# Optimization experiments

Measured on AMD Instinct MI355X. Metric: run time of the kernel, lower is better.

Reference implementation:

```python
import jax, jax.numpy as jnp
import numpy as np

B, TE, TD, H, D = 8, 2048, 256, 128, 128


def setup_inputs() -> dict:
    key = jax.random.key(0)
    k1, k2, k3, k4, k5 = jax.random.split(key, 5)
    he = lambda k, shape: jax.random.normal(k, shape, dtype=jnp.float32) * jnp.sqrt(2.0 / shape[0])
    return {
        "encoder_out_seq": jax.random.normal(k1, (B, TE, H), dtype=jnp.float32),
        "decoder_out_seq": jax.random.normal(k2, (B, TD, D), dtype=jnp.float32),
        "W_a": he(k3, (H, H)),
        "U_a": he(k4, (D, H)),
        "V_a": he(k5, (H, 1)),
    }


def reference(encoder_out_seq, decoder_out_seq, W_a, U_a, V_a):
    # Precompute encoder and decoder projections once (the TF code redundantly
    # recomputes enc@W_a every decoder step inside backend.rnn).
    Wenc = jnp.einsum('bth,hk->btk', encoder_out_seq, W_a)      # [B,Te,H]
    Udec = jnp.einsum('bjd,dk->bjk', decoder_out_seq, U_a)     # [B,Td,H]
    # Additive (Bahdanau) scores: v^T tanh(W s_i + U h_j)
    scores = jnp.einsum('bjtk,k->bjt',
                        jnp.tanh(Wenc[:, None, :, :] + Udec[:, :, None, :]),
                        V_a[:, 0])                              # [B,Td,Te]
    e_outputs = jax.nn.softmax(scores, axis=-1)                 # [B,Td,Te]
    c_outputs = jnp.einsum('bjt,bth->bjh', e_outputs, encoder_out_seq)  # [B,Td,H]
    return c_outputs, e_outputs
```

## Files before the change

kernel.cpp:

```cpp
#include <hip/hip_runtime.h>
#include <stdint.h>

#define B  8
#define TE 2048
#define TD 256
#define H  128

#define FMA4(acc, s, wv) \
  acc.x += (s)*(wv).x; acc.y += (s)*(wv).y; acc.z += (s)*(wv).z; acc.w += (s)*(wv).w

__global__ __launch_bounds__(256) void proj_kernel(
    const float* __restrict__ enc, const float* __restrict__ dec,
    const float* __restrict__ Wa,  const float* __restrict__ Ua,
    float* __restrict__ EgT, float* __restrict__ Fg) {
  __shared__ float Ls[16 * 132];
  const float C2 = 2.8853900817779268f;
  int tid = threadIdx.x;
  int bid = blockIdx.x;
  bool isE = (bid < 1024);
  int rbase = (isE ? bid : bid - 1024) * 16;
  const float* in = isE ? enc : dec;
  const float* Mg = isE ? Wa : Ua;
  int hq = tid & 31, rq = tid >> 5;
  int h0 = hq * 4, r0 = rq * 2;
  const float* rowp = in + (size_t)(rbase + r0) * H;
  const float* wp = Mg + h0;
  float4 a0{0,0,0,0}, a1{0,0,0,0};
  #pragma unroll 2
  for (int kb = 0; kb < 32; ++kb) {
    float4 rv0 = *(const float4*)(rowp + kb * 4);
    float4 rv1 = *(const float4*)(rowp + H + kb * 4);
    float4 w0 = *(const float4*)(wp + (size_t)(4 * kb + 0) * H);
    float4 w1 = *(const float4*)(wp + (size_t)(4 * kb + 1) * H);
    float4 w2 = *(const float4*)(wp + (size_t)(4 * kb + 2) * H);
    float4 w3 = *(const float4*)(wp + (size_t)(4 * kb + 3) * H);
    FMA4(a0, rv0.x, w0); FMA4(a0, rv0.y, w1); FMA4(a0, rv0.z, w2); FMA4(a0, rv0.w, w3);
    FMA4(a1, rv1.x, w0); FMA4(a1, rv1.y, w1); FMA4(a1, rv1.z, w2); FMA4(a1, rv1.w, w3);
  }
  float4 e0, e1;
  e0.x = __builtin_amdgcn_exp2f(a0.x * C2); e0.y = __builtin_amdgcn_exp2f(a0.y * C2);
  e0.z = __builtin_amdgcn_exp2f(a0.z * C2); e0.w = __builtin_amdgcn_exp2f(a0.w * C2);
  e1.x = __builtin_amdgcn_exp2f(a1.x * C2); e1.y = __builtin_amdgcn_exp2f(a1.y * C2);
  e1.z = __builtin_amdgcn_exp2f(a1.z * C2); e1.w = __builtin_amdgcn_exp2f(a1.w * C2);
  if (isE) {
    *(float4*)&Ls[(r0 + 0) * 132 + h0] = e0;
    *(float4*)&Ls[(r0 + 1) * 132 + h0] = e1;
    __syncthreads();
    int b_e = rbase >> 11, t_in = rbase & 2047;
    int tb = t_in >> 6, toff = t_in & 63;
    float* dst = EgT + (size_t)(b_e * 32 + tb) * 8192 + toff * 2;
    #pragma unroll
    for (int jj = 0; jj < 4; ++jj) {
      int idx = jj * 256 + tid;
      int r = idx & 15, q = idx >> 4;
      float2 val{Ls[r * 132 + 2 * q], Ls[r * 132 + 2 * q + 1]};
      *(float2*)(dst + (size_t)q * 128 + r * 2) = val;
    }
  } else {
    int b_f = rbase >> 8, j_in = rbase & 255;
    float* dst = Fg + ((size_t)(b_f * TD + j_in + r0)) * H + h0;
    *(float4*)(dst + 0 * H) = e0;
    *(float4*)(dst + 1 * H) = e1;
  }
}

__global__ __launch_bounds__(512, 4) void fused_kernel(
    const float* __restrict__ EgT, const float* __restrict__ Fg,
    const float* __restrict__ Va,  const float* __restrict__ enc,
    float* __restrict__ oute, float* __restrict__ outc) {
  __shared__ float S[4 * 2048];
  __shared__ float red[16];
  int tid = threadIdx.x;
  int bid = blockIdx.x;
  int b = bid & 7, jt = bid >> 3;
  int j0 = jt * 4;
  int lane = tid & 63, w = tid >> 6;
  const float4* vp = (const float4*)Va;
  float V1 = 0.f;
  #pragma unroll
  for (int q = 0; q < 32; ++q) { float4 v = vp[q]; V1 += v.x + v.y + v.z + v.w; }

  const float4* Fp = (const float4*)(Fg + (size_t)(b * TD + j0) * H);
  const float* Ep[4];
  #pragma unroll
  for (int it = 0; it < 4; ++it)
    Ep[it] = EgT + (size_t)(b * 32 + w + 8 * it) * 8192 + lane * 2;
  float s[4][4];
  #pragma unroll
  for (int it = 0; it < 4; ++it)
    #pragma unroll
    for (int j = 0; j < 4; ++j) s[it][j] = 0.f;
  float2 eka[4], ekb[4];

#define LOADE2(dst, base, off)                                       \
  { const float* _p = (base) + (off);                                \
    dst[0] = *(const float2*)(_p);       dst[1] = *(const float2*)(_p + 128);  \
    dst[2] = *(const float2*)(_p + 256); dst[3] = *(const float2*)(_p + 384); }

#define UNIT(acc, ekk, jj)                                                    \
  {                                                                           \
    float d0, d1, a = 0.f;                                                    \
    d0 = fmaf(ekk[0].x, f0[jj].x, 1.0f); d1 = fmaf(ekk[0].y, f0[jj].y, 1.0f); \
    a += (v0.x * d1 + v0.y * d0) * __builtin_amdgcn_rcpf(d0 * d1);            \
    d0 = fmaf(ekk[1].x, f0[jj].z, 1.0f); d1 = fmaf(ekk[1].y, f0[jj].w, 1.0f); \
    a += (v0.z * d1 + v0.w * d0) * __builtin_amdgcn_rcpf(d0 * d1);            \
    d0 = fmaf(ekk[2].x, f1[jj].x, 1.0f); d1 = fmaf(ekk[2].y, f1[jj].y, 1.0f); \
    a += (v1.x * d1 + v1.y * d0) * __builtin_amdgcn_rcpf(d0 * d1);            \
    d0 = fmaf(ekk[3].x, f1[jj].z, 1.0f); d1 = fmaf(ekk[3].y, f1[jj].w, 1.0f); \
    a += (v1.z * d1 + v1.w * d0) * __builtin_amdgcn_rcpf(d0 * d1);            \
    acc += a;                                                                 \
  }

  LOADE2(eka, Ep[0], 0);
  for (int kc = 0; kc < 16; ++kc) {
    float4 f0[4], f1[4];
    const float4* fpc = Fp + kc * 2;
    #pragma unroll
    for (int j = 0; j < 4; ++j) {
      f0[j] = fpc[j * 32];
      f1[j] = fpc[j * 32 + 1];
    }
    float4 v0 = vp[kc * 2], v1 = vp[kc * 2 + 1];
    LOADE2(ekb, Ep[1], kc * 512);
    #pragma unroll
    for (int j = 0; j < 4; ++j) UNIT(s[0][j], eka, j)
    LOADE2(eka, Ep[2], kc * 512);
    #pragma unroll
    for (int j = 0; j < 4; ++j) UNIT(s[1][j], ekb, j)
    LOADE2(ekb, Ep[3], kc * 512);
    #pragma unroll
    for (int j = 0; j < 4; ++j) UNIT(s[2][j], eka, j)
    LOADE2(eka, Ep[0], (kc + 1) * 512);
    #pragma unroll
    for (int j = 0; j < 4; ++j) UNIT(s[3][j], ekb, j)
  }
  #pragma unroll
  for (int it = 0; it < 4; ++it) {
    int t = (w + 8 * it) * 64 + lane;
    S[0 * 2048 + t] = V1 - 2.0f * s[it][0];
    S[1 * 2048 + t] = V1 - 2.0f * s[it][1];
    S[2 * 2048 + t] = V1 - 2.0f * s[it][2];
    S[3 * 2048 + t] = V1 - 2.0f * s[it][3];
  }
  __syncthreads();

  int j = w >> 1, half = w & 1;
  int tb2 = half * 1024 + lane;
  float x[16];
  #pragma unroll
  for (int q = 0; q < 16; ++q) x[q] = S[j * 2048 + tb2 + q * 64];
  float m = x[0];
  #pragma unroll
  for (int q = 1; q < 16; ++q) m = fmaxf(m, x[q]);
  #pragma unroll
  for (int off = 32; off > 0; off >>= 1) m = fmaxf(m, __shfl_xor(m, off));
  if (lane == 0) red[w] = m;
  __syncthreads();
  m = fmaxf(red[j * 2], red[j * 2 + 1]);
  const float L2E = 1.4426950408889634f;
  float sum = 0.f;
  #pragma unroll
  for (int q = 0; q < 16; ++q) {
    x[q] = __builtin_amdgcn_exp2f((x[q] - m) * L2E);
    sum += x[q];
  }
  #pragma unroll
  for (int off = 32; off > 0; off >>= 1) sum += __shfl_xor(sum, off);
  if (lane == 0) red[8 + w] = sum;
  __syncthreads();
  float inv = 1.0f / (red[8 + j * 2] + red[8 + j * 2 + 1]);
  float* orow = oute + (size_t)(b * TD + j0 + j) * TE;
  #pragma unroll
  for (int q = 0; q < 16; ++q) {
    float e = x[q] * inv;
    int t = tb2 + q * 64;
    orow[t] = e;
    S[j * 2048 + t] = e;
  }
  __syncthreads();

  int hq = tid & 31, slice = tid >> 5;
  const float* encp = enc + ((size_t)b * TE + slice * 128) * H + hq * 4;
  const float* Se = S + slice * 128;
  float4 ac0{0,0,0,0}, ac1{0,0,0,0}, ac2{0,0,0,0}, ac3{0,0,0,0};
  float4 evA0, evA1, evA2, evA3, evB0, evB1, evB2, evB3;

#define LOADENC(d0, d1, d2, d3, t0)                         \
  d0 = *(const float4*)(encp + (size_t)(t0 + 0) * H);       \
  d1 = *(const float4*)(encp + (size_t)(t0 + 1) * H);       \
  d2 = *(const float4*)(encp + (size_t)(t0 + 2) * H);       \
  d3 = *(const float4*)(encp + (size_t)(t0 + 3) * H);

#define GROUP(t0, ex, ey, ez, ew)                                            \
  {                                                                          \
    float4 E0 = *(const float4*)&Se[0 * 2048 + (t0)];                        \
    float4 E1 = *(const float4*)&Se[1 * 2048 + (t0)];                        \
    float4 E2 = *(const float4*)&Se[2 * 2048 + (t0)];                        \
    float4 E3 = *(const float4*)&Se[3 * 2048 + (t0)];                        \
    FMA4(ac0, E0.x, ex); FMA4(ac0, E0.y, ey); FMA4(ac0, E0.z, ez); FMA4(ac0, E0.w, ew); \
    FMA4(ac1, E1.x, ex); FMA4(ac1, E1.y, ey); FMA4(ac1, E1.z, ez); FMA4(ac1, E1.w, ew); \
    FMA4(ac2, E2.x, ex); FMA4(ac2, E2.y, ey); FMA4(ac2, E2.z, ez); FMA4(ac2, E2.w, ew); \
    FMA4(ac3, E3.x, ex); FMA4(ac3, E3.y, ey); FMA4(ac3, E3.z, ez); FMA4(ac3, E3.w, ew); \
  }

  LOADENC(evA0, evA1, evA2, evA3, 0);
  #pragma unroll
  for (int tb = 0; tb < 128; tb += 8) {
    LOADENC(evB0, evB1, evB2, evB3, tb + 4);
    GROUP(tb, evA0, evA1, evA2, evA3);
    if (tb < 120) { LOADENC(evA0, evA1, evA2, evA3, tb + 8); }
    GROUP(tb + 4, evB0, evB1, evB2, evB3);
  }
  __syncthreads();
  if (slice < 8) {
    float* dst = &S[slice * 512 + hq * 4];
    *(float4*)(dst + 0 * 128) = ac0; *(float4*)(dst + 1 * 128) = ac1;
    *(float4*)(dst + 2 * 128) = ac2; *(float4*)(dst + 3 * 128) = ac3;
  }
  __syncthreads();
  if (slice >= 8) {
    float* dst = &S[(slice - 8) * 512 + hq * 4];
    #define RMW(J, AC) { float4 p = *(float4*)(dst + J * 128); \
      p.x += AC.x; p.y += AC.y; p.z += AC.z; p.w += AC.w; \
      *(float4*)(dst + J * 128) = p; }
    RMW(0, ac0) RMW(1, ac1) RMW(2, ac2) RMW(3, ac3)
    #undef RMW
  }
  __syncthreads();
  float r = 0.f;
  #pragma unroll
  for (int sl = 0; sl < 8; ++sl) r += S[sl * 512 + tid];
  outc[(size_t)(b * TD + j0 + (tid >> 7)) * H + (tid & 127)] = r;
}

extern "C" void kernel_launch(void* const* d_in, const int* in_sizes, int n_in,
                              void* d_out, int out_size, void* d_ws, size_t ws_size,
                              hipStream_t stream) {
  (void)in_sizes; (void)n_in; (void)out_size; (void)ws_size;
  const float* enc = (const float*)d_in[0];
  const float* dec = (const float*)d_in[1];
  const float* Wa  = (const float*)d_in[2];
  const float* Ua  = (const float*)d_in[3];
  const float* Va  = (const float*)d_in[4];

  float* ws  = (float*)d_ws;
  float* EgT = ws;
  float* Fg  = EgT + (size_t)B * TE * H;
  float* outc = (float*)d_out;
  float* oute = outc + (size_t)B * TD * H;

  proj_kernel<<<dim3(1152), 256, 0, stream>>>(enc, dec, Wa, Ua, EgT, Fg);
  fused_kernel<<<dim3(512), 512, 0, stream>>>(EgT, Fg, Va, enc, oute, outc);
}
```

Baseline: 167.6 us.

## Merge four-term reciprocals into one rcp and double-buffer F loads

The inner score unit now combines four rational terms over a single common denominator, so it issues one reciprocal per four k-elements instead of two and folds the sum into one fma. The loop is also unrolled by two, with the F projection tile for the next chunk prefetched into a second register set while the current chunk is computed. Fewer transcendental ops and hidden load latency are the aim. The costs are higher register pressure, which may reduce occupancy, and a larger product of four denominators that could lose precision or overflow in extreme cases.

```diff
diff --git a/kernel.cpp b/kernel.cpp
--- a/kernel.cpp
+++ b/kernel.cpp
@@ -97,42 +97,61 @@
     dst[0] = *(const float2*)(_p);       dst[1] = *(const float2*)(_p + 128);  \
     dst[2] = *(const float2*)(_p + 256); dst[3] = *(const float2*)(_p + 384); }
 
-#define UNIT(acc, ekk, jj)                                                    \
-  {                                                                           \
-    float d0, d1, a = 0.f;                                                    \
-    d0 = fmaf(ekk[0].x, f0[jj].x, 1.0f); d1 = fmaf(ekk[0].y, f0[jj].y, 1.0f); \
-    a += (v0.x * d1 + v0.y * d0) * __builtin_amdgcn_rcpf(d0 * d1);            \
-    d0 = fmaf(ekk[1].x, f0[jj].z, 1.0f); d1 = fmaf(ekk[1].y, f0[jj].w, 1.0f); \
-    a += (v0.z * d1 + v0.w * d0) * __builtin_amdgcn_rcpf(d0 * d1);            \
-    d0 = fmaf(ekk[2].x, f1[jj].x, 1.0f); d1 = fmaf(ekk[2].y, f1[jj].y, 1.0f); \
-    a += (v1.x * d1 + v1.y * d0) * __builtin_amdgcn_rcpf(d0 * d1);            \
-    d0 = fmaf(ekk[3].x, f1[jj].z, 1.0f); d1 = fmaf(ekk[3].y, f1[jj].w, 1.0f); \
-    a += (v1.z * d1 + v1.w * d0) * __builtin_amdgcn_rcpf(d0 * d1);            \
-    acc += a;                                                                 \
-  }
-
+#define LOADF(d0, d1, kcv)                                           \
+  { const float4* fpc = Fp + (kcv) * 2;                              \
+    d0[0] = fpc[0];  d1[0] = fpc[1];                                 \
+    d0[1] = fpc[32]; d1[1] = fpc[33];                                \
+    d0[2] = fpc[64]; d1[2] = fpc[65];                                \
+    d0[3] = fpc[96]; d1[3] = fpc[97]; }
+
+#define UNIT4(accres, eA, eB, fv, vv)                                     \
+  {                                                                       \
+    float d0 = fmaf(eA.x, fv.x, 1.0f), d1 = fmaf(eA.y, fv.y, 1.0f);       \
+    float d2 = fmaf(eB.x, fv.z, 1.0f), d3 = fmaf(eB.y, fv.w, 1.0f);       \
+    float p01 = d0 * d1, p23 = d2 * d3;                                   \
+    float rP = __builtin_amdgcn_rcpf(p01 * p23);                          \
+    float n01 = vv.x * d1 + vv.y * d0;                                    \
+    float n23 = vv.z * d3 + vv.w * d2;                                    \
+    accres = fmaf(n01 * p23 + n23 * p01, rP, accres);                     \
+  }
+
+#define KCBODY(kcv, ff0, ff1)                                             \
+  {                                                                       \
+    float4 v0 = vp[(kcv) * 2], v1 = vp[(kcv) * 2 + 1];                    \
+    LOADE2(ekb, Ep[1], (kcv) * 512);                                      \
+    _Pragma("unroll")                                                     \
+    for (int j = 0; j < 4; ++j) {                                         \
+      UNIT4(s[0][j], eka[0], eka[1], ff0[j], v0);                         \
+      UNIT4(s[0][j], eka[2], eka[3], ff1[j], v1);                         \
+    }                                                                     \
+    LOADE2(eka, Ep[2], (kcv) * 512);                                      \
+    _Pragma("unroll")                                                     \
+    for (int j = 0; j < 4; ++j) {                                         \
+      UNIT4(s[1][j], ekb[0], ekb[1], ff0[j], v0);                         \
+      UNIT4(s[1][j], ekb[2], ekb[3], ff1[j], v1);                         \
+    }                                                                     \
+    LOADE2(ekb, Ep[3], (kcv) * 512);                                      \
+    _Pragma("unroll")                                                     \
+    for (int j = 0; j < 4; ++j) {                                         \
+      UNIT4(s[2][j], eka[0], eka[1], ff0[j], v0);                         \
+      UNIT4(s[2][j], eka[2], eka[3], ff1[j], v1);                         \
+    }                                                                     \
+    LOADE2(eka, Ep[0], ((kcv) + 1) * 512);   \
+    _Pragma("unroll")                                                     \
+    for (int j = 0; j < 4; ++j) {                                         \
+      UNIT4(s[3][j], ekb[0], ekb[1], ff0[j], v0);                         \
+      UNIT4(s[3][j], ekb[2], ekb[3], ff1[j], v1);                         \
+    }                                                                     \
+  }
+
+  float4 f0[4], f1[4], g0[4], g1[4];
+  LOADF(f0, f1, 0);
   LOADE2(eka, Ep[0], 0);
-  for (int kc = 0; kc < 16; ++kc) {
-    float4 f0[4], f1[4];
-    const float4* fpc = Fp + kc * 2;
-    #pragma unroll
-    for (int j = 0; j < 4; ++j) {
-      f0[j] = fpc[j * 32];
-      f1[j] = fpc[j * 32 + 1];
-    }
-    float4 v0 = vp[kc * 2], v1 = vp[kc * 2 + 1];
-    LOADE2(ekb, Ep[1], kc * 512);
-    #pragma unroll
-    for (int j = 0; j < 4; ++j) UNIT(s[0][j], eka, j)
-    LOADE2(eka, Ep[2], kc * 512);
-    #pragma unroll
-    for (int j = 0; j < 4; ++j) UNIT(s[1][j], ekb, j)
-    LOADE2(ekb, Ep[3], kc * 512);
-    #pragma unroll
-    for (int j = 0; j < 4; ++j) UNIT(s[2][j], eka, j)
-    LOADE2(eka, Ep[0], (kc + 1) * 512);
-    #pragma unroll
-    for (int j = 0; j < 4; ++j) UNIT(s[3][j], ekb, j)
+  for (int kc2 = 0; kc2 < 8; ++kc2) {
+    LOADF(g0, g1, 2 * kc2 + 1);
+    KCBODY(2 * kc2, f0, f1);
+    if (kc2 < 7) { LOADF(f0, f1, 2 * kc2 + 2); }
+    KCBODY(2 * kc2 + 1, g0, g1);
   }
   #pragma unroll
   for (int it = 0; it < 4; ++it) {
```

New measurement: 195.7 us. 16.8% more time.

## Halve decoder rows per block in fused attention kernel to double grid

Applied to the files above, without the earlier changes.

Each fused block now handles 2 decoder rows instead of 4, so the grid doubles to 1024 blocks and launch bounds ask for 8 blocks per CU. Shared memory and accumulator registers are halved, and the softmax is split across 4 waves per row. The aim is more parallelism and occupancy on a 512-block grid that may underfill the GPU. The cost is that each encoder-projection and encoder-value load is reused across only 2 rows, doubling global traffic for EgT and enc, and the tighter register cap may cause spills.

```diff
diff --git a/kernel.cpp b/kernel.cpp
--- a/kernel.cpp
+++ b/kernel.cpp
@@ -64,16 +64,16 @@
   }
 }
 
-__global__ __launch_bounds__(512, 4) void fused_kernel(
+__global__ __launch_bounds__(512, 8) void fused_kernel(
     const float* __restrict__ EgT, const float* __restrict__ Fg,
     const float* __restrict__ Va,  const float* __restrict__ enc,
     float* __restrict__ oute, float* __restrict__ outc) {
-  __shared__ float S[4 * 2048];
+  __shared__ float S[2 * 2048];
   __shared__ float red[16];
   int tid = threadIdx.x;
   int bid = blockIdx.x;
   int b = bid & 7, jt = bid >> 3;
-  int j0 = jt * 4;
+  int j0 = jt * 2;
   int lane = tid & 63, w = tid >> 6;
   const float4* vp = (const float4*)Va;
   float V1 = 0.f;
@@ -85,11 +85,9 @@
   #pragma unroll
   for (int it = 0; it < 4; ++it)
     Ep[it] = EgT + (size_t)(b * 32 + w + 8 * it) * 8192 + lane * 2;
-  float s[4][4];
-  #pragma unroll
-  for (int it = 0; it < 4; ++it)
-    #pragma unroll
-    for (int j = 0; j < 4; ++j) s[it][j] = 0.f;
+  float s[4][2];
+  #pragma unroll
+  for (int it = 0; it < 4; ++it) { s[it][0] = 0.f; s[it][1] = 0.f; }
   float2 eka[4], ekb[4];
 
 #define LOADE2(dst, base, off)                                       \
@@ -113,54 +111,48 @@
 
   LOADE2(eka, Ep[0], 0);
   for (int kc = 0; kc < 16; ++kc) {
-    float4 f0[4], f1[4];
+    float4 f0[2], f1[2];
     const float4* fpc = Fp + kc * 2;
     #pragma unroll
-    for (int j = 0; j < 4; ++j) {
+    for (int j = 0; j < 2; ++j) {
       f0[j] = fpc[j * 32];
       f1[j] = fpc[j * 32 + 1];
     }
     float4 v0 = vp[kc * 2], v1 = vp[kc * 2 + 1];
     LOADE2(ekb, Ep[1], kc * 512);
-    #pragma unroll
-    for (int j = 0; j < 4; ++j) UNIT(s[0][j], eka, j)
+    UNIT(s[0][0], eka, 0) UNIT(s[0][1], eka, 1)
     LOADE2(eka, Ep[2], kc * 512);
-    #pragma unroll
-    for (int j = 0; j < 4; ++j) UNIT(s[1][j], ekb, j)
+    UNIT(s[1][0], ekb, 0) UNIT(s[1][1], ekb, 1)
     LOADE2(ekb, Ep[3], kc * 512);
-    #pragma unroll
-    for (int j = 0; j < 4; ++j) UNIT(s[2][j], eka, j)
+    UNIT(s[2][0], eka, 0) UNIT(s[2][1], eka, 1)
     LOADE2(eka, Ep[0], (kc + 1) * 512);
-    #pragma unroll
-    for (int j = 0; j < 4; ++j) UNIT(s[3][j], ekb, j)
+    UNIT(s[3][0], ekb, 0) UNIT(s[3][1], ekb, 1)
   }
   #pragma unroll
   for (int it = 0; it < 4; ++it) {
     int t = (w + 8 * it) * 64 + lane;
     S[0 * 2048 + t] = V1 - 2.0f * s[it][0];
     S[1 * 2048 + t] = V1 - 2.0f * s[it][1];
-    S[2 * 2048 + t] = V1 - 2.0f * s[it][2];
-    S[3 * 2048 + t] = V1 - 2.0f * s[it][3];
-  }
-  __syncthreads();
-
-  int j = w >> 1, half = w & 1;
-  int tb2 = half * 1024 + lane;
-  float x[16];
-  #pragma unroll
-  for (int q = 0; q < 16; ++q) x[q] = S[j * 2048 + tb2 + q * 64];
+  }
+  __syncthreads();
+
+  int j = w >> 2, quarter = w & 3;
+  int tb2 = quarter * 512 + lane;
+  float x[8];
+  #pragma unroll
+  for (int q = 0; q < 8; ++q) x[q] = S[j * 2048 + tb2 + q * 64];
   float m = x[0];
   #pragma unroll
-  for (int q = 1; q < 16; ++q) m = fmaxf(m, x[q]);
+  for (int q = 1; q < 8; ++q) m = fmaxf(m, x[q]);
   #pragma unroll
   for (int off = 32; off > 0; off >>= 1) m = fmaxf(m, __shfl_xor(m, off));
   if (lane == 0) red[w] = m;
   __syncthreads();
-  m = fmaxf(red[j * 2], red[j * 2 + 1]);
+  m = fmaxf(fmaxf(red[j * 4], red[j * 4 + 1]), fmaxf(red[j * 4 + 2], red[j * 4 + 3]));
   const float L2E = 1.4426950408889634f;
   float sum = 0.f;
   #pragma unroll
-  for (int q = 0; q < 16; ++q) {
+  for (int q = 0; q < 8; ++q) {
     x[q] = __builtin_amdgcn_exp2f((x[q] - m) * L2E);
     sum += x[q];
   }
@@ -168,10 +160,11 @@
   for (int off = 32; off > 0; off >>= 1) sum += __shfl_xor(sum, off);
   if (lane == 0) red[8 + w] = sum;
   __syncthreads();
-  float inv = 1.0f / (red[8 + j * 2] + red[8 + j * 2 + 1]);
+  float inv = 1.0f / ((red[8 + j * 4] + red[8 + j * 4 + 1]) +
+                      (red[8 + j * 4 + 2] + red[8 + j * 4 + 3]));
   float* orow = oute + (size_t)(b * TD + j0 + j) * TE;
   #pragma unroll
-  for (int q = 0; q < 16; ++q) {
+  for (int q = 0; q < 8; ++q) {
     float e = x[q] * inv;
     int t = tb2 + q * 64;
     orow[t] = e;
@@ -182,7 +175,7 @@
   int hq = tid & 31, slice = tid >> 5;
   const float* encp = enc + ((size_t)b * TE + slice * 128) * H + hq * 4;
   const float* Se = S + slice * 128;
-  float4 ac0{0,0,0,0}, ac1{0,0,0,0}, ac2{0,0,0,0}, ac3{0,0,0,0};
+  float4 ac0{0,0,0,0}, ac1{0,0,0,0};
   float4 evA0, evA1, evA2, evA3, evB0, evB1, evB2, evB3;
 
 #define LOADENC(d0, d1, d2, d3, t0)                         \
@@ -195,12 +188,8 @@
   {                                                                          \
     float4 E0 = *(const float4*)&Se[0 * 2048 + (t0)];                        \
     float4 E1 = *(const float4*)&Se[1 * 2048 + (t0)];                        \
-    float4 E2 = *(const float4*)&Se[2 * 2048 + (t0)];                        \
-    float4 E3 = *(const float4*)&Se[3 * 2048 + (t0)];                        \
     FMA4(ac0, E0.x, ex); FMA4(ac0, E0.y, ey); FMA4(ac0, E0.z, ez); FMA4(ac0, E0.w, ew); \
     FMA4(ac1, E1.x, ex); FMA4(ac1, E1.y, ey); FMA4(ac1, E1.z, ez); FMA4(ac1, E1.w, ew); \
-    FMA4(ac2, E2.x, ex); FMA4(ac2, E2.y, ey); FMA4(ac2, E2.z, ez); FMA4(ac2, E2.w, ew); \
-    FMA4(ac3, E3.x, ex); FMA4(ac3, E3.y, ey); FMA4(ac3, E3.z, ez); FMA4(ac3, E3.w, ew); \
   }
 
   LOADENC(evA0, evA1, evA2, evA3, 0);
@@ -213,24 +202,26 @@
   }
   __syncthreads();
   if (slice < 8) {
-    float* dst = &S[slice * 512 + hq * 4];
-    *(float4*)(dst + 0 * 128) = ac0; *(float4*)(dst + 1 * 128) = ac1;
-    *(float4*)(dst + 2 * 128) = ac2; *(float4*)(dst + 3 * 128) = ac3;
+    float* dst = &S[slice * 256 + hq * 4];
+    *(float4*)(dst + 0)   = ac0;
+    *(float4*)(dst + 128) = ac1;
   }
   __syncthreads();
   if (slice >= 8) {
-    float* dst = &S[(slice - 8) * 512 + hq * 4];
-    #define RMW(J, AC) { float4 p = *(float4*)(dst + J * 128); \
+    float* dst = &S[(slice - 8) * 256 + hq * 4];
+    #define RMW(OFF, AC) { float4 p = *(float4*)(dst + OFF); \
       p.x += AC.x; p.y += AC.y; p.z += AC.z; p.w += AC.w; \
-      *(float4*)(dst + J * 128) = p; }
-    RMW(0, ac0) RMW(1, ac1) RMW(2, ac2) RMW(3, ac3)
+      *(float4*)(dst + OFF) = p; }
+    RMW(0, ac0) RMW(128, ac1)
     #undef RMW
   }
   __syncthreads();
-  float r = 0.f;
-  #pragma unroll
-  for (int sl = 0; sl < 8; ++sl) r += S[sl * 512 + tid];
-  outc[(size_t)(b * TD + j0 + (tid >> 7)) * H + (tid & 127)] = r;
+  if (tid < 256) {
+    float r = 0.f;
+    #pragma unroll
+    for (int sl = 0; sl < 8; ++sl) r += S[sl * 256 + tid];
+    outc[(size_t)(b * TD + j0 + (tid >> 7)) * H + (tid & 127)] = r;
+  }
 }
 
 extern "C" void kernel_launch(void* const* d_in, const int* in_sizes, int n_in,
@@ -250,5 +241,5 @@
   float* oute = outc + (size_t)B * TD * H;
 
   proj_kernel<<<dim3(1152), 256, 0, stream>>>(enc, dec, Wa, Ua, EgT, Fg);
-  fused_kernel<<<dim3(512), 512, 0, stream>>>(EgT, Fg, Va, enc, oute, outc);
+  fused_kernel<<<dim3(1024), 512, 0, stream>>>(EgT, Fg, Va, enc, oute, outc);
 }
```

After: 202.2 us. 20.7% more time.
